# Kernel tuning notes

Measured on AMD Instinct MI355X. Metric: run time of the kernel, lower is better.

Reference implementation:

```python
import jax, jax.numpy as jnp
import numpy as np

B, N, D, DFF, E, K, H = 8, 1024, 512, 2048, 8, 2, 8


def setup_inputs() -> dict:
    key = jax.random.key(0)
    ks = jax.random.split(key, 20)
    p = lambda k, shape: (jax.random.normal(k, shape, jnp.float32) * 0.02)
    x = jax.random.normal(ks[0], (B, N, D), jnp.float32)
    adj = (jax.random.uniform(ks[1], (B, N, N)) > 0.5).astype(jnp.float32)
    return {
        "x": x,
        "adj": adj,
        "gc_w": p(ks[2], (D, D)),
        "gc_b": jnp.zeros((D,), jnp.float32),
        "root_emb": p(ks[3], (1, D)),
        "in_w": p(ks[4], (3 * D, D)),
        "in_b": jnp.zeros((3 * D,), jnp.float32),
        "out_w": p(ks[5], (D, D)),
        "out_b": jnp.zeros((D,), jnp.float32),
        "ln1_g": jnp.ones((D,), jnp.float32),
        "ln1_b": jnp.zeros((D,), jnp.float32),
        "ln2_g": jnp.ones((D,), jnp.float32),
        "ln2_b": jnp.zeros((D,), jnp.float32),
        "gate_w": p(ks[6], (E, D)),
        "W1": p(ks[7], (E, D, DFF)),
        "b1": jnp.zeros((E, DFF), jnp.float32),
        "W2": p(ks[8], (E, DFF, D)),
        "b2": jnp.zeros((E, D), jnp.float32),
    }


def layer_norm(x, g, b, eps=1e-5):
    mu = jnp.mean(x, axis=-1, keepdims=True)
    var = jnp.var(x, axis=-1, keepdims=True)
    return (x - mu) * jax.lax.rsqrt(var + eps) * g + b


def reference(x, adj, gc_w, gc_b, root_emb, in_w, in_b, out_w, out_b,
              ln1_g, ln1_b, ln2_g, ln2_b, gate_w, W1, b1, W2, b2):
    b, n, d = x.shape
    h = H
    hd = d // h
    # GraphConv: adj @ x -> linear -> + root embedding (index 0 for every batch)
    g = jnp.einsum('bij,bjd->bid', adj, x) @ gc_w.T + gc_b + root_emb[0]
    x = x + g
    # MultiheadAttention (self-attn, eval mode, no mask)
    qkv = x @ in_w.T + in_b                      # [B,N,3D]
    q, k, v = jnp.split(qkv, 3, axis=-1)
    to_heads = lambda t: t.reshape(b, n, h, hd).transpose(0, 2, 1, 3)
    q, k, v = to_heads(q), to_heads(k), to_heads(v)
    scale = jnp.float32(1.0) / jnp.sqrt(jnp.float32(hd))
    scores = jnp.einsum('bhqe,bhke->bhqk', q * scale, k)
    attn = jax.nn.softmax(scores, axis=-1)
    o = jnp.einsum('bhqk,bhke->bhqe', attn, v).transpose(0, 2, 1, 3).reshape(b, n, d)
    o = o @ out_w.T + out_b
    x = layer_norm(x + o, ln1_g, ln1_b)
    # MoE: top-k gating, normalized weights, weighted sum of expert FFN outputs
    xf = x.reshape(-1, d)                        # [T,D]
    t = xf.shape[0]
    gate_probs = jax.nn.softmax(xf @ gate_w.T, axis=-1)        # [T,E]
    topk_p, topk_i = jax.lax.top_k(gate_probs, K)
    topk_p = topk_p / jnp.sum(topk_p, axis=-1, keepdims=True)
    num_e = gate_w.shape[0]
    w = jnp.zeros((t, num_e), xf.dtype).at[jnp.arange(t)[:, None], topk_i].add(topk_p)
    hid = jax.nn.gelu(jnp.einsum('td,edf->etf', xf, W1) + b1[:, None, :], approximate=False)
    y = jnp.einsum('etf,efd->etd', hid, W2) + b2[:, None, :]   # [E,T,D]
    moe = jnp.einsum('te,etd->td', w, y).reshape(b, n, d)
    return layer_norm(x + moe, ln2_g, ln2_b)
```

## Files before the change

### kernel.cpp

```cpp
#include <hip/hip_runtime.h>
#include <hip/hip_bf16.h>

#define NB 8
#define NSEQ 1024
#define DMODEL 512
#define DF 2048
#define NEXP 8
#define NHEAD 8
#define HDIM 64
#define T_TOK (NB * NSEQ)

typedef unsigned short u16;
typedef float f32x4_t __attribute__((ext_vector_type(4)));
typedef __bf16 bf16x8_t __attribute__((ext_vector_type(8)));

__device__ __forceinline__ u16 f2b(float f) {
  __hip_bfloat16 h = __float2bfloat16(f);
  return *reinterpret_cast<u16*>(&h);
}
__device__ __forceinline__ float b2f(u16 u) {
  return __uint_as_float((unsigned)u << 16);
}
__device__ __forceinline__ void gl_lds16(const u16* g, u16* l) {
  __builtin_amdgcn_global_load_lds(
      (const __attribute__((address_space(1))) unsigned int*)g,
      (__attribute__((address_space(3))) unsigned int*)l, 16, 0, 0);
}

__global__ __launch_bounds__(256) void k_cvt_hl(const float* __restrict__ src,
                                                u16* __restrict__ hi,
                                                u16* __restrict__ lo, int n4) {
  const int i = blockIdx.x * 256 + threadIdx.x;
  if (i >= n4) return;
  const float4 v = ((const float4*)src)[i];
  ushort4 h, l;
  h.x = f2b(v.x); l.x = f2b(v.x - b2f(h.x));
  h.y = f2b(v.y); l.y = f2b(v.y - b2f(h.y));
  h.z = f2b(v.z); l.z = f2b(v.z - b2f(h.z));
  h.w = f2b(v.w); l.w = f2b(v.w - b2f(h.w));
  ((ushort4*)hi)[i] = h;
  ((ushort4*)lo)[i] = l;
}

__global__ __launch_bounds__(256) void k_cvt_b(const float* __restrict__ src,
                                               u16* __restrict__ dst, int n4) {
  const int i = blockIdx.x * 256 + threadIdx.x;
  if (i >= n4) return;
  const float4 v = ((const float4*)src)[i];
  ushort4 h;
  h.x = f2b(v.x); h.y = f2b(v.y); h.z = f2b(v.z); h.w = f2b(v.w);
  ((ushort4*)dst)[i] = h;
}

__global__ __launch_bounds__(256) void k_cvt_t_hl(const float* __restrict__ src,
                                                  u16* __restrict__ hi,
                                                  u16* __restrict__ lo,
                                                  int R, int C) {
  const int z = blockIdx.z;
  src += (size_t)z * R * C;
  hi += (size_t)z * R * C;
  lo += (size_t)z * R * C;
  const int r0 = blockIdx.y * 64, c0 = blockIdx.x * 64;
  __shared__ u16 th[64][65], tl[64][65];
  const int t = threadIdx.x;
  const int cc = t & 63, rb = t >> 6;
#pragma unroll
  for (int i = 0; i < 16; ++i) {
    const int r = i * 4 + rb;
    const float f = src[(size_t)(r0 + r) * C + c0 + cc];
    const u16 h = f2b(f);
    th[r][cc] = h;
    tl[r][cc] = f2b(f - b2f(h));
  }
  __syncthreads();
#pragma unroll
  for (int i = 0; i < 16; ++i) {
    const int r = i * 4 + rb;
    hi[(size_t)(c0 + r) * R + r0 + cc] = th[cc][r];
    lo[(size_t)(c0 + r) * R + r0 + cc] = tl[cc][r];
  }
}

template <int TERMS, int EP>
__global__ __launch_bounds__(256) void k_gemm_sp(
    const u16* __restrict__ Ah, const u16* __restrict__ Al,
    const u16* __restrict__ Bh, const u16* __restrict__ Bl,
    const float* __restrict__ bias, const float* __restrict__ addv,
    const float* __restrict__ addm, float* __restrict__ outF,
    u16* __restrict__ outH, u16* __restrict__ outL,
    u16* __restrict__ outVH, u16* __restrict__ outVL, int K, int N,
    size_t aStride, size_t bStride, size_t cStride) {
  const int z = blockIdx.z;
  Ah += (size_t)z * aStride;
  if (TERMS == 3) Al += (size_t)z * aStride;
  Bh += (size_t)z * bStride;
  Bl += (size_t)z * bStride;
  const int m0 = blockIdx.y * 128, n0 = blockIdx.x * 128;
  __shared__ u16 Ash[128][64];
  __shared__ u16 Asl[(TERMS == 3) ? 128 : 1][64];
  __shared__ u16 Bsh[128][64];
  __shared__ u16 Bsl[128][64];
  const int t = threadIdx.x;
  const int w = t >> 6, l = t & 63;
  const int srow = w * 8 + (l >> 3);
  const int sscol = ((l & 7) ^ (l >> 3)) * 8;
  size_t aoff[4], boff[4];
#pragma unroll
  for (int i = 0; i < 4; ++i) {
    aoff[i] = (size_t)(m0 + i * 32 + srow) * K + sscol;
    boff[i] = (size_t)(n0 + i * 32 + srow) * K + sscol;
  }
  const int wr = w >> 1, wc = w & 1;
  const int lr = l & 15, lg = l >> 4;
  f32x4_t acc[4][4] = {};
  for (int k0 = 0; k0 < K; k0 += 64) {
#pragma unroll
    for (int i = 0; i < 4; ++i) {
      gl_lds16(Ah + aoff[i] + k0, &Ash[i * 32 + w * 8][0]);
      if (TERMS == 3) gl_lds16(Al + aoff[i] + k0, &Asl[i * 32 + w * 8][0]);
      gl_lds16(Bh + boff[i] + k0, &Bsh[i * 32 + w * 8][0]);
      gl_lds16(Bl + boff[i] + k0, &Bsl[i * 32 + w * 8][0]);
    }
    __syncthreads();
#pragma unroll
    for (int kk = 0; kk < 2; ++kk) {
      const int cs = (kk * 32 + lg * 8) ^ ((lr & 7) << 3);
      bf16x8_t ah[4], al[4], bh[4], bl[4];
#pragma unroll
      for (int m = 0; m < 4; ++m) {
        ah[m] = *(const bf16x8_t*)&Ash[wr * 64 + m * 16 + lr][cs];
        if (TERMS == 3)
          al[m] = *(const bf16x8_t*)&Asl[wr * 64 + m * 16 + lr][cs];
      }
#pragma unroll
      for (int n = 0; n < 4; ++n) {
        bh[n] = *(const bf16x8_t*)&Bsh[wc * 64 + n * 16 + lr][cs];
        bl[n] = *(const bf16x8_t*)&Bsl[wc * 64 + n * 16 + lr][cs];
      }
#pragma unroll
      for (int m = 0; m < 4; ++m)
#pragma unroll
        for (int n = 0; n < 4; ++n) {
          acc[m][n] = __builtin_amdgcn_mfma_f32_16x16x32_bf16(ah[m], bh[n],
                                                              acc[m][n], 0, 0, 0);
          acc[m][n] = __builtin_amdgcn_mfma_f32_16x16x32_bf16(ah[m], bl[n],
                                                              acc[m][n], 0, 0, 0);
          if (TERMS == 3)
            acc[m][n] = __builtin_amdgcn_mfma_f32_16x16x32_bf16(
                al[m], bh[n], acc[m][n], 0, 0, 0);
        }
    }
    __syncthreads();
  }
  const size_t cb = (size_t)z * cStride;
#pragma unroll
  for (int m = 0; m < 4; ++m) {
#pragma unroll
    for (int n = 0; n < 4; ++n) {
      const int c = n0 + wc * 64 + n * 16 + lr;
#pragma unroll
      for (int j = 0; j < 4; ++j) {
        const int r = m0 + wr * 64 + m * 16 + lg * 4 + j;
        float v = acc[m][n][j];
        if (EP == 1) v += bias[c] + addv[c] + addm[(size_t)r * N + c];
        if (EP == 2 || EP == 4) v += bias[c];
        const size_t idx = cb + (size_t)r * N + c;
        if (EP == 1 || EP == 2) outF[idx] = v;
        if (EP == 0 || EP == 1) {
          const u16 h = f2b(v);
          outH[idx] = h;
          outL[idx] = f2b(v - b2f(h));
        }
        if (EP == 4) {
          if (c < DMODEL) v *= 0.125f;
          const u16 h = f2b(v);
          const u16 lo = f2b(v - b2f(h));
          if (c < 2 * DMODEL) {
            outH[idx] = h;
            outL[idx] = lo;
          } else {
            const int d = (c - 2 * DMODEL) & 63;
            const int hd = (c - 2 * DMODEL) >> 6;
            const int bb = r >> 10;
            const int tile = (r & 1023) >> 6;
            const int tv = r & 63;
            const int cc2 = 4 * (tv & 15) + (tv >> 4);
            const int stc = cc2 ^ ((d & 7) << 3);
            const size_t vo =
                (((size_t)(bb * 8 + hd) * 16 + tile) * 64 + d) * 64 + stc;
            outVH[vo] = h;
            outVL[vo] = lo;
          }
        }
      }
    }
  }
}

__global__ __launch_bounds__(256) void k_attn(const u16* __restrict__ qh_g,
                                              const u16* __restrict__ ql_g,
                                              const u16* __restrict__ vph,
                                              const u16* __restrict__ vpl,
                                              u16* __restrict__ oh_g,
                                              u16* __restrict__ ol_g) {
  const int q0 = blockIdx.x * 128, h = blockIdx.y, b = blockIdx.z;
  const int t = threadIdx.x;
  const int w = t >> 6, l = t & 63;
  const int lr = l & 15, lg = l >> 4;
  __shared__ u16 Ksh[64][64], Ksl[64][64];
  __shared__ u16 Vth[64][64], Vtl[64][64];
  __shared__ u16 Psh[128][64], Psl[128][64];
  u16* VthF = &Vth[0][0];
  u16* VtlF = &Vtl[0][0];
  bf16x8_t qh[2][2], ql[2][2];
#pragma unroll
  for (int s = 0; s < 2; ++s) {
    const size_t qoff =
        (size_t)(b * NSEQ + q0 + s * 64 + w * 16 + lr) * (3 * DMODEL) +
        h * HDIM;
#pragma unroll
    for (int kc = 0; kc < 2; ++kc) {
      qh[s][kc] = *(const bf16x8_t*)(qh_g + qoff + kc * 32 + lg * 8);
      ql[s][kc] = *(const bf16x8_t*)(ql_g + qoff + kc * 32 + lg * 8);
    }
  }
  float mrow[2][4], lrow[2][4];
#pragma unroll
  for (int s = 0; s < 2; ++s)
#pragma unroll
    for (int j = 0; j < 4; ++j) { mrow[s][j] = -1e30f; lrow[s][j] = 0.f; }
  f32x4_t acc_o[2][4] = {};
  const int sr = t >> 2;
  const int sc = (t & 3) * 16;
  const int cs0 = sc ^ ((sr & 7) << 3);
  const int cs1 = (sc + 8) ^ ((sr & 7) << 3);
  const size_t vbh = ((size_t)(b * 8 + h) * 16) * 4096;
  const int vsub = w * 512 + l * 8;
  uint4 pkh0, pkh1, pkl0, pkl1, pvh0, pvh1, pvl0, pvl1;
  {
    const size_t kro =
        (size_t)(b * NSEQ + sr) * (3 * DMODEL) + DMODEL + h * HDIM + sc;
    pkh0 = *(const uint4*)(qh_g + kro);
    pkh1 = *(const uint4*)(qh_g + kro + 8);
    pkl0 = *(const uint4*)(ql_g + kro);
    pkl1 = *(const uint4*)(ql_g + kro + 8);
    pvh0 = *(const uint4*)(vph + vbh + vsub);
    pvh1 = *(const uint4*)(vph + vbh + 2048 + vsub);
    pvl0 = *(const uint4*)(vpl + vbh + vsub);
    pvl1 = *(const uint4*)(vpl + vbh + 2048 + vsub);
  }
  for (int k0 = 0; k0 < NSEQ; k0 += 64) {
    __syncthreads();
    *(uint4*)&Ksh[sr][cs0] = pkh0;
    *(uint4*)&Ksh[sr][cs1] = pkh1;
    *(uint4*)&Ksl[sr][cs0] = pkl0;
    *(uint4*)&Ksl[sr][cs1] = pkl1;
    *(uint4*)(VthF + vsub) = pvh0;
    *(uint4*)(VthF + 2048 + vsub) = pvh1;
    *(uint4*)(VtlF + vsub) = pvl0;
    *(uint4*)(VtlF + 2048 + vsub) = pvl1;
    __syncthreads();
    if (k0 + 64 < NSEQ) {
      const size_t kro = (size_t)(b * NSEQ + k0 + 64 + sr) * (3 * DMODEL) +
                         DMODEL + h * HDIM + sc;
      pkh0 = *(const uint4*)(qh_g + kro);
      pkh1 = *(const uint4*)(qh_g + kro + 8);
      pkl0 = *(const uint4*)(ql_g + kro);
      pkl1 = *(const uint4*)(ql_g + kro + 8);
      const size_t vt = vbh + (size_t)((k0 >> 6) + 1) * 4096;
      pvh0 = *(const uint4*)(vph + vt + vsub);
      pvh1 = *(const uint4*)(vph + vt + 2048 + vsub);
      pvl0 = *(const uint4*)(vpl + vt + vsub);
      pvl1 = *(const uint4*)(vpl + vt + 2048 + vsub);
    }
    f32x4_t sacc[2][4] = {};
    __builtin_amdgcn_s_setprio(1);
#pragma unroll
    for (int kc = 0; kc < 2; ++kc) {
      const int cs = (kc * 32 + lg * 8) ^ ((lr & 7) << 3);
#pragma unroll
      for (int n = 0; n < 4; ++n) {
        const bf16x8_t kh = *(const bf16x8_t*)&Ksh[n * 16 + lr][cs];
        const bf16x8_t kl = *(const bf16x8_t*)&Ksl[n * 16 + lr][cs];
#pragma unroll
        for (int s = 0; s < 2; ++s) {
          sacc[s][n] = __builtin_amdgcn_mfma_f32_16x16x32_bf16(
              qh[s][kc], kh, sacc[s][n], 0, 0, 0);
          sacc[s][n] = __builtin_amdgcn_mfma_f32_16x16x32_bf16(
              qh[s][kc], kl, sacc[s][n], 0, 0, 0);
          sacc[s][n] = __builtin_amdgcn_mfma_f32_16x16x32_bf16(
              ql[s][kc], kh, sacc[s][n], 0, 0, 0);
        }
      }
    }
    __builtin_amdgcn_s_setprio(0);
#pragma unroll
    for (int s = 0; s < 2; ++s) {
      float alpha[4];
#pragma unroll
      for (int j = 0; j < 4; ++j) {
        float mx = fmaxf(fmaxf(sacc[s][0][j], sacc[s][1][j]),
                         fmaxf(sacc[s][2][j], sacc[s][3][j]));
        mx = fmaxf(mx, __shfl_xor(mx, 1));
        mx = fmaxf(mx, __shfl_xor(mx, 2));
        mx = fmaxf(mx, __shfl_xor(mx, 4));
        mx = fmaxf(mx, __shfl_xor(mx, 8));
        const float mnew = fmaxf(mrow[s][j], mx);
        alpha[j] = __expf(mrow[s][j] - mnew);
        mrow[s][j] = mnew;
        float psum = 0.f;
        const int prow = lg * 4 + j;
        ushort4 ph4, pl4;
        u16* php = (u16*)&ph4;
        u16* plp = (u16*)&pl4;
#pragma unroll
        for (int n = 0; n < 4; ++n) {
          const float p = __expf(sacc[s][n][j] - mnew);
          psum += p;
          const u16 hi = f2b(p);
          php[n] = hi;
          plp[n] = f2b(p - b2f(hi));
        }
        const int pc = (4 * lr) ^ ((prow & 7) << 3);
        *(ushort4*)&Psh[s * 64 + w * 16 + prow][pc] = ph4;
        *(ushort4*)&Psl[s * 64 + w * 16 + prow][pc] = pl4;
        psum += __shfl_xor(psum, 1);
        psum += __shfl_xor(psum, 2);
        psum += __shfl_xor(psum, 4);
        psum += __shfl_xor(psum, 8);
        lrow[s][j] = lrow[s][j] * alpha[j] + psum;
      }
#pragma unroll
      for (int n = 0; n < 4; ++n)
#pragma unroll
        for (int j = 0; j < 4; ++j) acc_o[s][n][j] *= alpha[j];
    }
    __builtin_amdgcn_s_setprio(1);
#pragma unroll
    for (int kc = 0; kc < 2; ++kc) {
      const int cs = (kc * 32 + lg * 8) ^ ((lr & 7) << 3);
      bf16x8_t ph[2], pl[2];
#pragma unroll
      for (int s = 0; s < 2; ++s) {
        ph[s] = *(const bf16x8_t*)&Psh[s * 64 + w * 16 + lr][cs];
        pl[s] = *(const bf16x8_t*)&Psl[s * 64 + w * 16 + lr][cs];
      }
#pragma unroll
      for (int n = 0; n < 4; ++n) {
        const bf16x8_t vh = *(const bf16x8_t*)&Vth[n * 16 + lr][cs];
        const bf16x8_t vl = *(const bf16x8_t*)&Vtl[n * 16 + lr][cs];
#pragma unroll
        for (int s = 0; s < 2; ++s) {
          acc_o[s][n] = __builtin_amdgcn_mfma_f32_16x16x32_bf16(
              ph[s], vh, acc_o[s][n], 0, 0, 0);
          acc_o[s][n] = __builtin_amdgcn_mfma_f32_16x16x32_bf16(
              ph[s], vl, acc_o[s][n], 0, 0, 0);
          acc_o[s][n] = __builtin_amdgcn_mfma_f32_16x16x32_bf16(
              pl[s], vh, acc_o[s][n], 0, 0, 0);
        }
      }
    }
    __builtin_amdgcn_s_setprio(0);
  }
#pragma unroll
  for (int s = 0; s < 2; ++s) {
#pragma unroll
    for (int j = 0; j < 4; ++j) {
      const float invl = 1.0f / lrow[s][j];
      const size_t ro =
          (size_t)(b * NSEQ + q0 + s * 64 + w * 16 + lg * 4 + j) * DMODEL +
          h * HDIM;
#pragma unroll
      for (int n = 0; n < 4; ++n) {
        const float v = acc_o[s][n][j] * invl;
        const u16 hh = f2b(v);
        oh_g[ro + n * 16 + lr] = hh;
        ol_g[ro + n * 16 + lr] = f2b(v - b2f(hh));
      }
    }
  }
}

__global__ __launch_bounds__(256) void k_ln_add(
    const float* __restrict__ a, const float* __restrict__ bsrc,
    const float* __restrict__ g, const float* __restrict__ be,
    const float* __restrict__ gw, float* __restrict__ outp,
    u16* __restrict__ outb, int* __restrict__ eidx,
    float* __restrict__ ewgt) {
  const int tok = blockIdx.x;
  const int t = threadIdx.x;
  float2 v;
  {
    const float2 va = *(const float2*)(a + (size_t)tok * DMODEL + t * 2);
    const float2 vb = *(const float2*)(bsrc + (size_t)tok * DMODEL + t * 2);
    v.x = va.x + vb.x; v.y = va.y + vb.y;
  }
  float s1 = v.x + v.y, s2 = v.x * v.x + v.y * v.y;
#pragma unroll
  for (int o = 32; o; o >>= 1) { s1 += __shfl_down(s1, o); s2 += __shfl_down(s2, o); }
  __shared__ float sm1[4], sm2[4];
  __shared__ float smg[4][NEXP];
  if ((t & 63) == 0) { sm1[t >> 6] = s1; sm2[t >> 6] = s2; }
  __syncthreads();
  s1 = sm1[0] + sm1[1] + sm1[2] + sm1[3];
  s2 = sm2[0] + sm2[1] + sm2[2] + sm2[3];
  const float mean = s1 * (1.f / DMODEL);
  const float var = s2 * (1.f / DMODEL) - mean * mean;
  const float rstd = rsqrtf(var + 1e-5f);
  float2 o;
  o.x = (v.x - mean) * rstd * g[t * 2] + be[t * 2];
  o.y = (v.y - mean) * rstd * g[t * 2 + 1] + be[t * 2 + 1];
  *(float2*)(outp + (size_t)tok * DMODEL + t * 2) = o;
  ushort2 ob;
  ob.x = f2b(o.x); ob.y = f2b(o.y);
  *(ushort2*)(outb + (size_t)tok * DMODEL + t * 2) = ob;
  float p[NEXP];
#pragma unroll
  for (int e = 0; e < NEXP; ++e) {
    const float2 wv = *(const float2*)(gw + e * DMODEL + t * 2);
    p[e] = o.x * wv.x + o.y * wv.y;
  }
#pragma unroll
  for (int e = 0; e < NEXP; ++e) {
    p[e] += __shfl_xor(p[e], 1);
    p[e] += __shfl_xor(p[e], 2);
    p[e] += __shfl_xor(p[e], 4);
    p[e] += __shfl_xor(p[e], 8);
    p[e] += __shfl_xor(p[e], 16);
    p[e] += __shfl_xor(p[e], 32);
  }
  if ((t & 63) == 0) {
#pragma unroll
    for (int e = 0; e < NEXP; ++e) smg[t >> 6][e] = p[e];
  }
  __syncthreads();
  if (t == 0) {
    float lg2[NEXP];
#pragma unroll
    for (int e = 0; e < NEXP; ++e)
      lg2[e] = smg[0][e] + smg[1][e] + smg[2][e] + smg[3][e];
    int i0 = 0; float b0 = lg2[0];
#pragma unroll
    for (int e = 1; e < NEXP; ++e) if (lg2[e] > b0) { b0 = lg2[e]; i0 = e; }
    int i1 = -1; float v1 = -1e30f;
#pragma unroll
    for (int e = 0; e < NEXP; ++e)
      if (e != i0 && lg2[e] > v1) { v1 = lg2[e]; i1 = e; }
    const float tt = __expf(v1 - b0);
    const float w0 = 1.f / (1.f + tt), w1 = tt / (1.f + tt);
    eidx[tok * 2] = i0; eidx[tok * 2 + 1] = i1;
    ewgt[tok * 2] = w0; ewgt[tok * 2 + 1] = w1;
  }
}

__global__ void k_zero(int* __restrict__ p, int n) {
  const int i = blockIdx.x * blockDim.x + threadIdx.x;
  if (i < n) p[i] = 0;
}

__global__ __launch_bounds__(256) void k_count(const int* __restrict__ eidx,
                                               int* __restrict__ ecnt) {
  __shared__ int cnt[NEXP];
  const int t = threadIdx.x;
  if (t < NEXP) cnt[t] = 0;
  __syncthreads();
  atomicAdd(&cnt[eidx[blockIdx.x * 256 + t]], 1);
  __syncthreads();
  if (t < NEXP) atomicAdd(&ecnt[t], cnt[t]);
}

__global__ void k_offsets(const int* __restrict__ ecnt,
                          int* __restrict__ eoff, int* __restrict__ blkmap) {
  if (threadIdx.x == 0) {
    int s = 0;
    for (int e = 0; e < NEXP; ++e) { eoff[e] = s; s += ecnt[e]; }
    int nb = 0;
    for (int e = 0; e < NEXP; ++e)
      for (int m0 = 0; m0 < ecnt[e]; m0 += 128)
        blkmap[1 + nb++] = e | (m0 << 4);
    blkmap[0] = nb;
  }
}

__global__ __launch_bounds__(256) void k_scatter(
    const int* __restrict__ eidx, const int* __restrict__ eoff,
    int* __restrict__ efill, int* __restrict__ rtok, int* __restrict__ t2s) {
  __shared__ int lcnt[NEXP];
  __shared__ int lbase[NEXP];
  const int t = threadIdx.x;
  if (t < NEXP) lcnt[t] = 0;
  __syncthreads();
  const int tok = blockIdx.x * 128 + (t >> 1);
  const int k = t & 1;
  const int e = eidx[tok * 2 + k];
  const int lpos = atomicAdd(&lcnt[e], 1);
  __syncthreads();
  if (t < NEXP) lbase[t] = atomicAdd(&efill[t], lcnt[t]);
  __syncthreads();
  const int slot = eoff[e] + lbase[e] + lpos;
  rtok[slot] = tok;
  t2s[tok * 2 + k] = slot;
}

__global__ __launch_bounds__(256) void k_cvt_t(const float* __restrict__ src,
                                               u16* __restrict__ dst,
                                               int R, int C) {
  const int e = blockIdx.z;
  src += (size_t)e * R * C;
  dst += (size_t)e * R * C;
  const int r0 = blockIdx.y * 64, c0 = blockIdx.x * 64;
  __shared__ u16 tile[64][65];
  const int t = threadIdx.x;
  const int cc = t & 63, rb = t >> 6;
#pragma unroll
  for (int i = 0; i < 16; ++i) {
    const int r = i * 4 + rb;
    tile[r][cc] = f2b(src[(size_t)(r0 + r) * C + c0 + cc]);
  }
  __syncthreads();
#pragma unroll
  for (int i = 0; i < 16; ++i) {
    const int r = i * 4 + rb;
    dst[(size_t)(c0 + r) * R + r0 + cc] = tile[cc][r];
  }
}

template <int MODE>
__global__ __launch_bounds__(256) void k_moe_mfma(
    const u16* __restrict__ Ab, const u16* __restrict__ Bb,
    const float* __restrict__ bias, const int* __restrict__ rtok,
    const int* __restrict__ ecnt, const int* __restrict__ eoff,
    const int* __restrict__ blkmap, u16* __restrict__ outp) {
  constexpr int K = (MODE == 0) ? DMODEL : DF;
  constexpr int N = (MODE == 0) ? DF : DMODEL;
  const int nb = blkmap[0];
  if ((int)blockIdx.y >= nb) return;
  const int ent = blkmap[1 + blockIdx.y];
  const int e = ent & 15;
  const int m0 = ent >> 4;
  const int cnt = ecnt[e];
  const int off = eoff[e];
  const int n0 = blockIdx.x * 128;
  const u16* Bw = Bb + (size_t)e * (size_t)K * N;
  __shared__ u16 As[128][64];
  __shared__ u16 Bs[128][64];
  const int t = threadIdx.x;
  const int w = t >> 6, l = t & 63;
  const int srow = w * 8 + (l >> 3);
  const int sscol = ((l & 7) ^ (l >> 3)) * 8;
  const u16* arow[4];
#pragma unroll
  for (int i = 0; i < 4; ++i) {
    const int r = m0 + i * 32 + srow;
    const int rr = (r < cnt) ? r : (cnt - 1);
    if (MODE == 0)
      arow[i] = Ab + (size_t)rtok[off + rr] * K + sscol;
    else
      arow[i] = Ab + ((size_t)off + rr) * K + sscol;
  }
  const u16* brow[4];
#pragma unroll
  for (int i = 0; i < 4; ++i)
    brow[i] = Bw + (size_t)(n0 + i * 32 + srow) * K + sscol;

  const int wr = w >> 1, wc = w & 1;
  const int lr = l & 15, lg = l >> 4;
  f32x4_t acc[4][4] = {};
  for (int k0 = 0; k0 < K; k0 += 64) {
#pragma unroll
    for (int i = 0; i < 4; ++i) {
      gl_lds16(arow[i] + k0, &As[i * 32 + w * 8][0]);
      gl_lds16(brow[i] + k0, &Bs[i * 32 + w * 8][0]);
    }
    __syncthreads();
#pragma unroll
    for (int kk = 0; kk < 2; ++kk) {
      const int cs = (kk * 32 + lg * 8) ^ ((lr & 7) << 3);
      bf16x8_t af[4], bfr[4];
#pragma unroll
      for (int m = 0; m < 4; ++m)
        af[m] = *(const bf16x8_t*)&As[wr * 64 + m * 16 + lr][cs];
#pragma unroll
      for (int n = 0; n < 4; ++n)
        bfr[n] = *(const bf16x8_t*)&Bs[wc * 64 + n * 16 + lr][cs];
#pragma unroll
      for (int m = 0; m < 4; ++m)
#pragma unroll
        for (int n = 0; n < 4; ++n)
          acc[m][n] = __builtin_amdgcn_mfma_f32_16x16x32_bf16(
              af[m], bfr[n], acc[m][n], 0, 0, 0);
    }
    __syncthreads();
  }
#pragma unroll
  for (int m = 0; m < 4; ++m) {
    const int rl0 = wr * 64 + m * 16 + lg * 4;
#pragma unroll
    for (int n = 0; n < 4; ++n) {
      const int gc = n0 + wc * 64 + n * 16 + lr;
      const float bv = bias[e * N + gc];
#pragma unroll
      for (int j = 0; j < 4; ++j) {
        const int r = m0 + rl0 + j;
        if (r < cnt) {
          float v = acc[m][n][j] + bv;
          if (MODE == 0) v = v * 0.5f * (1.f + erff(v * 0.70710678118f));
          outp[((size_t)off + r) * N + gc] = f2b(v);
        }
      }
    }
  }
}

__global__ __launch_bounds__(256) void k_ln2(
    const float* __restrict__ x2, const u16* __restrict__ ybuf,
    const int* __restrict__ t2s, const float* __restrict__ ewgt,
    const float* __restrict__ g, const float* __restrict__ be,
    float* __restrict__ outp) {
  const int tok = blockIdx.x;
  const int t = threadIdx.x;
  const int s0 = t2s[tok * 2], s1i = t2s[tok * 2 + 1];
  const float w0 = ewgt[tok * 2], w1 = ewgt[tok * 2 + 1];
  float2 v;
  {
    const float2 a = *(const float2*)(x2 + (size_t)tok * DMODEL + t * 2);
    const ushort2 y0 = *(const ushort2*)(ybuf + (size_t)s0 * DMODEL + t * 2);
    const ushort2 y1 = *(const ushort2*)(ybuf + (size_t)s1i * DMODEL + t * 2);
    v.x = a.x + w0 * b2f(y0.x) + w1 * b2f(y1.x);
    v.y = a.y + w0 * b2f(y0.y) + w1 * b2f(y1.y);
  }
  float sum1 = v.x + v.y, sum2 = v.x * v.x + v.y * v.y;
#pragma unroll
  for (int o = 32; o; o >>= 1) { sum1 += __shfl_down(sum1, o); sum2 += __shfl_down(sum2, o); }
  __shared__ float sm1[4], sm2[4];
  if ((t & 63) == 0) { sm1[t >> 6] = sum1; sm2[t >> 6] = sum2; }
  __syncthreads();
  sum1 = sm1[0] + sm1[1] + sm1[2] + sm1[3];
  sum2 = sm2[0] + sm2[1] + sm2[2] + sm2[3];
  const float mean = sum1 * (1.f / DMODEL);
  const float var = sum2 * (1.f / DMODEL) - mean * mean;
  const float rstd = rsqrtf(var + 1e-5f);
  float2 o;
  o.x = (v.x - mean) * rstd * g[t * 2] + be[t * 2];
  o.y = (v.y - mean) * rstd * g[t * 2 + 1] + be[t * 2 + 1];
  *(float2*)(outp + (size_t)tok * DMODEL + t * 2) = o;
}

extern "C" void kernel_launch(void* const* d_in, const int* in_sizes, int n_in,
                              void* d_out, int out_size, void* d_ws,
                              size_t ws_size, hipStream_t stream) {
  const float* x      = (const float*)d_in[0];
  const float* adj    = (const float*)d_in[1];
  const float* gc_w   = (const float*)d_in[2];
  const float* gc_b   = (const float*)d_in[3];
  const float* root   = (const float*)d_in[4];
  const float* in_w   = (const float*)d_in[5];
  const float* in_b   = (const float*)d_in[6];
  const float* out_w  = (const float*)d_in[7];
  const float* out_b  = (const float*)d_in[8];
  const float* ln1_g  = (const float*)d_in[9];
  const float* ln1_b  = (const float*)d_in[10];
  const float* ln2_g  = (const float*)d_in[11];
  const float* ln2_b  = (const float*)d_in[12];
  const float* gate_w = (const float*)d_in[13];
  const float* W1     = (const float*)d_in[14];
  const float* b1     = (const float*)d_in[15];
  const float* W2     = (const float*)d_in[16];
  const float* b2     = (const float*)d_in[17];
  float* outp = (float*)d_out;

  constexpr size_t MB = 1ull << 20;
  char* W = (char*)d_ws;
  u16*   adj_bf = (u16*)(W + 0);
  u16*   xht    = (u16*)(W + 16 * MB);
  u16*   xlt    = (u16*)(W + 24 * MB);
  u16*   axh    = (u16*)(W + 32 * MB);
  u16*   axl    = (u16*)(W + 40 * MB);
  float* x1     = (float*)(W + 48 * MB);
  u16*   x1h    = (u16*)(W + 64 * MB);
  u16*   x1l    = (u16*)(W + 72 * MB);
  u16*   qkvh   = (u16*)(W + 0);
  u16*   qkvl   = (u16*)(W + 24 * MB);
  u16*   vph    = (u16*)(W + 80 * MB);
  u16*   vpl    = (u16*)(W + 88 * MB);
  u16*   oatth  = (u16*)(W + 96 * MB);
  u16*   oattl  = (u16*)(W + 104 * MB);
  float* oproj  = (float*)(W + 0);
  float* x2     = (float*)(W + 96 * MB);
  u16*   Wxb    = (u16*)(W + 80 * MB);
  u16*   hid    = (u16*)(W + 16 * MB);
  u16*   ybuf   = (u16*)(W + 0);
  char*  misc   = W + 112 * MB;
  char*  Od     = (char*)d_out;
  u16*   gwh = (u16*)(Od + 0);
  u16*   gwl = (u16*)(Od + 512 * 1024);
  u16*   iwh = (u16*)(Od + 1 * MB);
  u16*   iwl = (u16*)(Od + 1 * MB + 1536 * 1024);
  u16*   owh = (u16*)(Od + 4 * MB);
  u16*   owl = (u16*)(Od + 4 * MB + 512 * 1024);
  u16*   x2b = (u16*)d_out;
  int*   eidx  = (int*)misc;
  float* ewgt  = (float*)(misc + 65536);
  int*   ecnt  = (int*)(misc + 131072);
  int*   eoff  = (int*)(misc + 131072 + 128);
  int*   efill = (int*)(misc + 131072 + 256);
  int*   rtok  = (int*)(misc + 131072 + 512);
  int*   t2s   = (int*)(misc + 131072 + 512 + 65536);
  int*   blkmap = (int*)(misc + 131072 + 512 + 131072);

  k_cvt_b<<<dim3(8192), 256, 0, stream>>>(adj, adj_bf, NB * NSEQ * NSEQ / 4);
  k_cvt_t_hl<<<dim3(8, 16, 8), 256, 0, stream>>>(x, xht, xlt, NSEQ, DMODEL);
  k_cvt_hl<<<dim3(256), 256, 0, stream>>>(gc_w, gwh, gwl, DMODEL * DMODEL / 4);
  k_cvt_hl<<<dim3(768), 256, 0, stream>>>(in_w, iwh, iwl, 3 * DMODEL * DMODEL / 4);
  k_cvt_hl<<<dim3(256), 256, 0, stream>>>(out_w, owh, owl, DMODEL * DMODEL / 4);
  k_gemm_sp<2, 0><<<dim3(4, 8, 8), 256, 0, stream>>>(
      adj_bf, nullptr, xht, xlt, nullptr, nullptr, nullptr, nullptr, axh, axl,
      nullptr, nullptr, NSEQ, DMODEL, (size_t)NSEQ * NSEQ,
      (size_t)DMODEL * NSEQ, (size_t)NSEQ * DMODEL);
  k_gemm_sp<3, 1><<<dim3(4, 64, 1), 256, 0, stream>>>(
      axh, axl, gwh, gwl, gc_b, root, x, x1, x1h, x1l, nullptr, nullptr,
      DMODEL, DMODEL, 0, 0, 0);
  k_gemm_sp<3, 4><<<dim3(12, 64, 1), 256, 0, stream>>>(
      x1h, x1l, iwh, iwl, in_b, nullptr, nullptr, nullptr, qkvh, qkvl, vph,
      vpl, DMODEL, 3 * DMODEL, 0, 0, 0);
  k_attn<<<dim3(8, 8, 8), 256, 0, stream>>>(qkvh, qkvl, vph, vpl, oatth,
                                            oattl);
  k_gemm_sp<3, 2><<<dim3(4, 64, 1), 256, 0, stream>>>(
      oatth, oattl, owh, owl, out_b, nullptr, nullptr, oproj, nullptr, nullptr,
      nullptr, nullptr, DMODEL, DMODEL, 0, 0, 0);
  k_ln_add<<<dim3(T_TOK), 256, 0, stream>>>(x1, oproj, ln1_g, ln1_b, gate_w,
                                            x2, x2b, eidx, ewgt);
  k_zero<<<dim3(1), 128, 0, stream>>>((int*)(misc + 131072), 128);
  k_count<<<dim3(2 * T_TOK / 256), 256, 0, stream>>>(eidx, ecnt);
  k_offsets<<<dim3(1), 64, 0, stream>>>(ecnt, eoff, blkmap);
  k_scatter<<<dim3(T_TOK / 128), 256, 0, stream>>>(eidx, eoff, efill, rtok,
                                                   t2s);
  k_cvt_t<<<dim3(DF / 64, DMODEL / 64, NEXP), 256, 0, stream>>>(W1, Wxb,
                                                                DMODEL, DF);
  k_moe_mfma<0><<<dim3(DF / 128, 135, 1), 256, 0, stream>>>(
      x2b, Wxb, b1, rtok, ecnt, eoff, blkmap, hid);
  k_cvt_t<<<dim3(DMODEL / 64, DF / 64, NEXP), 256, 0, stream>>>(W2, Wxb, DF,
                                                                DMODEL);
  k_moe_mfma<1><<<dim3(DMODEL / 128, 135, 1), 256, 0, stream>>>(
      hid, Wxb, b2, rtok, ecnt, eoff, blkmap, ybuf);
  k_ln2<<<dim3(T_TOK), 256, 0, stream>>>(x2, ybuf, t2s, ewgt, ln2_g, ln2_b,
                                         outp);
}
```

Measured before the change: 497.8 us.

## Double-buffer LDS tiles in MoE MFMA GEMM to overlap loads with compute

Result: no change. 498.1 us (+0.1%).

```diff
diff --git a/kernel.cpp b/kernel.cpp
--- a/kernel.cpp
+++ b/kernel.cpp
@@ -542,8 +542,8 @@
   const int off = eoff[e];
   const int n0 = blockIdx.x * 128;
   const u16* Bw = Bb + (size_t)e * (size_t)K * N;
-  __shared__ u16 As[128][64];
-  __shared__ u16 Bs[128][64];
+  __shared__ u16 As[2][128][64];
+  __shared__ u16 Bs[2][128][64];
   const int t = threadIdx.x;
   const int w = t >> 6, l = t & 63;
   const int srow = w * 8 + (l >> 3);
@@ -566,23 +566,41 @@
   const int wr = w >> 1, wc = w & 1;
   const int lr = l & 15, lg = l >> 4;
   f32x4_t acc[4][4] = {};
+#pragma unroll
+  for (int i = 0; i < 4; ++i) {
+    gl_lds16(arow[i], &As[0][i * 32 + w * 8][0]);
+    gl_lds16(brow[i], &Bs[0][i * 32 + w * 8][0]);
+  }
+  asm volatile("s_waitcnt vmcnt(0)" ::: "memory");
+  __builtin_amdgcn_sched_barrier(0);
+  __builtin_amdgcn_s_barrier();
+  __builtin_amdgcn_sched_barrier(0);
+  int cur = 0;
   for (int k0 = 0; k0 < K; k0 += 64) {
-#pragma unroll
-    for (int i = 0; i < 4; ++i) {
-      gl_lds16(arow[i] + k0, &As[i * 32 + w * 8][0]);
-      gl_lds16(brow[i] + k0, &Bs[i * 32 + w * 8][0]);
-    }
-    __syncthreads();
+    const bool has_next = (k0 + 64 < K);
+    if (has_next) {
+#pragma unroll
+      for (int i = 0; i < 4; ++i) {
+        gl_lds16(arow[i] + k0 + 64, &As[cur ^ 1][i * 32 + w * 8][0]);
+        gl_lds16(brow[i] + k0 + 64, &Bs[cur ^ 1][i * 32 + w * 8][0]);
+      }
+      asm volatile("s_waitcnt vmcnt(8)" ::: "memory");
+    } else {
+      asm volatile("s_waitcnt vmcnt(0)" ::: "memory");
+    }
+    __builtin_amdgcn_sched_barrier(0);
+    __builtin_amdgcn_s_barrier();
+    __builtin_amdgcn_sched_barrier(0);
 #pragma unroll
     for (int kk = 0; kk < 2; ++kk) {
       const int cs = (kk * 32 + lg * 8) ^ ((lr & 7) << 3);
       bf16x8_t af[4], bfr[4];
 #pragma unroll
       for (int m = 0; m < 4; ++m)
-        af[m] = *(const bf16x8_t*)&As[wr * 64 + m * 16 + lr][cs];
+        af[m] = *(const bf16x8_t*)&As[cur][wr * 64 + m * 16 + lr][cs];
 #pragma unroll
       for (int n = 0; n < 4; ++n)
-        bfr[n] = *(const bf16x8_t*)&Bs[wc * 64 + n * 16 + lr][cs];
+        bfr[n] = *(const bf16x8_t*)&Bs[cur][wc * 64 + n * 16 + lr][cs];
 #pragma unroll
       for (int m = 0; m < 4; ++m)
 #pragma unroll
@@ -590,7 +608,10 @@
           acc[m][n] = __builtin_amdgcn_mfma_f32_16x16x32_bf16(
               af[m], bfr[n], acc[m][n], 0, 0, 0);
     }
-    __syncthreads();
+    __builtin_amdgcn_sched_barrier(0);
+    __builtin_amdgcn_s_barrier();
+    __builtin_amdgcn_sched_barrier(0);
+    cur ^= 1;
   }
 #pragma unroll
   for (int m = 0; m < 4; ++m) {
```
